# Kernel optimization log

Hardware: AMD Instinct MI355X
Metric: run time of the kernel (lower is better)

The kernel has to match this reference:

```python
import jax, jax.numpy as jnp
import numpy as np

BETA = 0.25


def setup_inputs() -> dict:
    key = jax.random.key(0)
    k1, k2 = jax.random.split(key)
    x = jax.random.normal(k1, (4, 4096, 256), dtype=jnp.float32)
    emb = jax.random.normal(k2, (8192, 256), dtype=jnp.float32)
    return {"x": x, "emb": emb}


def reference(x, emb):
    B, C, D = x.shape
    xf = x.reshape(-1, D)  # [B*C, D]
    # squared euclidean distances (argmin-equivalent to torch.cdist p=2)
    # dist2[i, n] = ||xf_i||^2 - 2 xf_i . e_n + ||e_n||^2
    dist2 = (
        jnp.sum(xf * xf, axis=-1, keepdims=True)
        - 2.0 * jnp.einsum("td,nd->tn", xf, emb)
        + jnp.sum(emb * emb, axis=-1)[None, :]
    )  # [B*C, N]
    idx = jnp.argmin(dist2, axis=-1)  # [B*C]
    quant = emb[idx]  # [B*C, D]
    commitment_loss = jnp.mean((jax.lax.stop_gradient(quant) - xf) ** 2)
    codebook_loss = jnp.mean((quant - jax.lax.stop_gradient(xf)) ** 2)
    quantize_loss = codebook_loss + BETA * commitment_loss
    # straight-through estimator
    quant_out = xf + jax.lax.stop_gradient(quant - xf)
    quant_out = quant_out.reshape(B, C, D)
    indices = idx.reshape(B, C)
    return quant_out, quantize_loss, indices
```

## Files before the change

kernel.cpp:

```cpp
#include <hip/hip_runtime.h>
#include <stdint.h>

#define T_ROWS 16384
#define D_DIM  256
#define N_CODES 8192
#define NSPLIT 4
#define NS (N_CODES / NSPLIT)
#define NCHUNK (NS / 128)
#define NITER (NCHUNK * 8)

typedef _Float16 h8v __attribute__((ext_vector_type(8)));
typedef float f4v __attribute__((ext_vector_type(4)));
typedef unsigned short u16;
typedef unsigned int u32;
typedef unsigned long long u64;

typedef const __attribute__((address_space(1))) uint32_t* as1_t;
typedef __attribute__((address_space(3))) uint32_t* as3_t;

__device__ __forceinline__ void gload_lds16(const void* g, void* l) {
    __builtin_amdgcn_global_load_lds((as1_t)(uintptr_t)g, (as3_t)(uintptr_t)l, 16, 0, 0);
}
__device__ __forceinline__ u32 umin32(u32 a, u32 b) { return a < b ? a : b; }
__device__ __forceinline__ u32 umax32(u32 a, u32 b) { return a > b ? a : b; }

__global__ void k_prep_emb(const float* __restrict__ emb, u16* __restrict__ Ef,
                           float* __restrict__ enormP) {
    int wv = threadIdx.x >> 6, lane = threadIdx.x & 63;
    int row = blockIdx.x * 4 + wv;
    float4 v = *reinterpret_cast<const float4*>(emb + (size_t)row * D_DIM + lane * 4);
    float s = v.x * v.x + v.y * v.y + v.z * v.z + v.w * v.w;
    ushort4 h;
    { _Float16 t0=(_Float16)v.x,t1=(_Float16)v.y,t2=(_Float16)v.z,t3=(_Float16)v.w;
      h.x=*reinterpret_cast<u16*>(&t0); h.y=*reinterpret_cast<u16*>(&t1);
      h.z=*reinterpret_cast<u16*>(&t2); h.w=*reinterpret_cast<u16*>(&t3); }
    reinterpret_cast<ushort4*>(Ef + (size_t)row * D_DIM)[lane] = h;
#pragma unroll
    for (int off = 32; off; off >>= 1) s += __shfl_xor(s, off, 64);
    if (lane == 0) enormP[row] = s + 1024.0f;
}

__global__ __launch_bounds__(256, 2)
void k_main_mfma(const float* __restrict__ x, const u16* __restrict__ Ef,
                 const float* __restrict__ enormP, u32* __restrict__ cand) {
    __shared__ u16 Bs[3][4096];

    const int tid = threadIdx.x;
    const int lane = tid & 63;
    const int w = tid >> 6;
    const int c15 = lane & 15, grp = lane >> 4;
    const int m0 = (int)(blockIdx.x >> 2) * 128;
    const int split = (int)(blockIdx.x & 3);
    const int nbase = split * NS;

    int boff[8];
#pragma unroll
    for (int ni = 0; ni < 8; ++ni) {
        int r = ni * 16 + c15;
        boff[ni] = (r * 64 + grp * 16) ^ (((r >> 1) & 3) << 4);
    }
    const int srow = tid >> 2;
    const int kkb = ((tid & 3) ^ ((srow >> 1) & 3)) * 8;

    h8v a[2][8];
#pragma unroll
    for (int mi = 0; mi < 2; ++mi)
#pragma unroll
        for (int ks = 0; ks < 8; ++ks) {
            const float* p = x + (size_t)(m0 + w * 32 + mi * 16 + c15) * D_DIM + ks * 32 + grp * 8;
            float4 u0 = *reinterpret_cast<const float4*>(p);
            float4 u1 = *reinterpret_cast<const float4*>(p + 4);
            h8v av;
            av[0] = (_Float16)u0.x; av[1] = (_Float16)u0.y;
            av[2] = (_Float16)u0.z; av[3] = (_Float16)u0.w;
            av[4] = (_Float16)u1.x; av[5] = (_Float16)u1.y;
            av[6] = (_Float16)u1.z; av[7] = (_Float16)u1.w;
            a[mi][ks] = av;
        }

    auto stageB = [&](int buf, int it) {
        const int nc = it >> 3, ks = it & 7;
        const u16* src = Ef + (size_t)(nbase + nc * 128 + srow) * D_DIM + ks * 32 + kkb;
        gload_lds16(src, (char*)Bs + buf * 8192 + tid * 16);
        gload_lds16(src + 64 * D_DIM, (char*)Bs + buf * 8192 + 4096 + tid * 16);
    };

    u32 b1[8], b2[8];
#pragma unroll
    for (int l = 0; l < 8; ++l) { b1[l] = 0xFFFFFFFFu; b2[l] = 0xFFFFFFFFu; }

    stageB(0, 0);
    stageB(1, 1);
    asm volatile("s_waitcnt vmcnt(2)\n\ts_barrier" ::: "memory");

    f4v acc[2][8];
    float en[8];
    int rb = 0;

    for (int nc = 0; nc < NCHUNK; ++nc) {
#pragma unroll
        for (int ni = 0; ni < 8; ++ni)
            en[ni] = enormP[nbase + nc * 128 + ni * 16 + c15];
#pragma unroll
        for (int mi = 0; mi < 2; ++mi)
#pragma unroll
            for (int ni = 0; ni < 8; ++ni) acc[mi][ni] = f4v{0.f, 0.f, 0.f, 0.f};

#pragma unroll
        for (int ks = 0; ks < 8; ++ks) {
            const int it = nc * 8 + ks;
            const int wb = rb >= 1 ? rb - 1 : 2;
            if (it < NITER - 2) stageB(wb, it + 2);

            h8v b[8];
            const char* bsb = (const char*)Bs + rb * 8192;
#pragma unroll
            for (int ni = 0; ni < 8; ++ni)
                b[ni] = *reinterpret_cast<const h8v*>(bsb + boff[ni]);

            __builtin_amdgcn_s_setprio(1);
#pragma unroll
            for (int mi = 0; mi < 2; ++mi)
#pragma unroll
                for (int ni = 0; ni < 8; ++ni)
                    acc[mi][ni] = __builtin_amdgcn_mfma_f32_16x16x32_f16(
                        a[mi][ks], b[ni], acc[mi][ni], 0, 0, 0);
            __builtin_amdgcn_s_setprio(0);

            if (ks == 7) {
#pragma unroll
                for (int mi = 0; mi < 2; ++mi)
#pragma unroll
                    for (int r = 0; r < 4; ++r) {
                        const int l = mi * 4 + r;
                        u32 kmin = 0xFFFFFFFFu;
#pragma unroll
                        for (int ni = 0; ni < 8; ++ni) {
                            float s = fmaf(-2.0f, acc[mi][ni][r], en[ni]);
                            u32 k = (__float_as_uint(s) & 0xFFFFF800u)
                                  | (u32)(nc * 128 + ni * 16 + c15);
                            kmin = umin32(kmin, k);
                        }
                        b2[l] = umin32(b2[l], umax32(b1[l], kmin));
                        b1[l] = umin32(b1[l], kmin);
                    }
            }

            if (it < NITER - 2)
                asm volatile("s_waitcnt vmcnt(2)\n\ts_barrier" ::: "memory");
            else if (it == NITER - 2)
                asm volatile("s_waitcnt vmcnt(0)\n\ts_barrier" ::: "memory");
            rb = rb < 2 ? rb + 1 : 0;
        }
    }

#pragma unroll
    for (int l = 0; l < 8; ++l) {
#pragma unroll
        for (int off = 1; off < 16; off <<= 1) {
            u32 o1 = __shfl_xor(b1[l], off, 64);
            u32 o2 = __shfl_xor(b2[l], off, 64);
            b2[l] = umin32(umax32(b1[l], o1), umin32(b2[l], o2));
            b1[l] = umin32(b1[l], o1);
        }
    }
    if (c15 == 0) {
#pragma unroll
        for (int mi = 0; mi < 2; ++mi)
#pragma unroll
            for (int r = 0; r < 4; ++r) {
                const int l = mi * 4 + r;
                const int grow = m0 + w * 32 + mi * 16 + grp * 4 + r;
                cand[grow * 8 + split * 2 + 0] = (u32)nbase + (b1[l] & 0x7FFu);
                cand[grow * 8 + split * 2 + 1] = (u32)nbase + (b2[l] & 0x7FFu);
            }
    }
}

__global__ void k_refine(const float* __restrict__ x, const float* __restrict__ emb,
                         const u32* __restrict__ cand, float* __restrict__ out,
                         double* __restrict__ partials) {
    const int tid = threadIdx.x;
    const int wv = tid >> 6, lane = tid & 63;
    const int row = blockIdx.x * 4 + wv;
    const int cslot = lane >> 3, sub = lane & 7;
    int idx = (int)cand[row * 8 + cslot];
    double d = 0.0;
#pragma unroll
    for (int j = 0; j < 8; ++j) {
        float4 xv = *reinterpret_cast<const float4*>(x + (size_t)row * D_DIM + sub * 32 + j * 4);
        float4 ev = *reinterpret_cast<const float4*>(emb + (size_t)idx * D_DIM + sub * 32 + j * 4);
        double d0 = (double)xv.x - (double)ev.x;
        double d1 = (double)xv.y - (double)ev.y;
        double d2 = (double)xv.z - (double)ev.z;
        double d3 = (double)xv.w - (double)ev.w;
        d += d0 * d0 + d1 * d1 + d2 * d2 + d3 * d3;
    }
#pragma unroll
    for (int off = 1; off < 8; off <<= 1) d += __shfl_xor(d, off, 64);
#pragma unroll
    for (int off = 8; off < 64; off <<= 1) {
        double od = __shfl_xor(d, off, 64);
        int oi = __shfl_xor(idx, off, 64);
        bool better = (od < d) || (od == d && oi < idx);
        d = better ? od : d;
        idx = better ? oi : idx;
    }
    if (lane == 0) {
        out[(size_t)T_ROWS * D_DIM + 1 + row] = (float)idx;
        partials[row] = d;
    }
    float4 e = *reinterpret_cast<const float4*>(emb + (size_t)idx * D_DIM + lane * 4);
    *reinterpret_cast<float4*>(out + (size_t)row * D_DIM + lane * 4) = e;
}

__global__ void k_loss_d(const double* __restrict__ partials, float* __restrict__ out) {
    double s = 0.0;
    const int t = threadIdx.x;
#pragma unroll
    for (int i = 0; i < 64; ++i) s += partials[t + 256 * i];
#pragma unroll
    for (int off = 32; off; off >>= 1) s += __shfl_xor(s, off, 64);
    __shared__ double sm[4];
    const int wv = t >> 6, lane = t & 63;
    if (lane == 0) sm[wv] = s;
    __syncthreads();
    if (t == 0) {
        const double tot = sm[0] + sm[1] + sm[2] + sm[3];
        out[(size_t)T_ROWS * D_DIM] = (float)(1.25 * tot / (double)((size_t)T_ROWS * D_DIM));
    }
}

__global__ void k_enorm(const float* __restrict__ emb, float* __restrict__ enorm) {
    int wave = threadIdx.x >> 6, lane = threadIdx.x & 63;
    int row = blockIdx.x * 4 + wave;
    float4 v = *reinterpret_cast<const float4*>(emb + (size_t)row * D_DIM + lane * 4);
    float s = v.x * v.x + v.y * v.y + v.z * v.z + v.w * v.w;
#pragma unroll
    for (int off = 32; off; off >>= 1) s += __shfl_xor(s, off, 64);
    if (lane == 0) enorm[row] = s;
}

__global__ void k_init(u64* __restrict__ keys) {
    keys[blockIdx.x * blockDim.x + threadIdx.x] = ~0ull;
}

__global__ __launch_bounds__(256, 2)
void k_main_fp32(const float* __restrict__ x, const float* __restrict__ emb,
                 const float* __restrict__ enorm, u64* __restrict__ keys) {
    __shared__ float Xs[32][128];
    __shared__ float Es[32][128];
    __shared__ u64 red[128][16];

    const int tid = threadIdx.x;
    const int tx = tid & 15, ty = tid >> 4;
    const int m0 = (blockIdx.x >> 2) * 128;
    const int nbase = (blockIdx.x & 3) * (N_CODES / 4);

    float best[8];
    int bidx[8];
#pragma unroll
    for (int r = 0; r < 8; ++r) { best[r] = 3.4e38f; bidx[r] = 0; }

    for (int nc = 0; nc < (N_CODES / 4) / 128; ++nc) {
        const int n0 = nbase + nc * 128;
        float acc[8][8] = {};
        for (int k0 = 0; k0 < D_DIM; k0 += 32) {
            __syncthreads();
            {
                const int m = tid & 127, q = tid >> 7;
#pragma unroll
                for (int i = 0; i < 4; ++i) {
                    const int k4 = q * 4 + i * 8;
                    float4 v = *reinterpret_cast<const float4*>(
                        x + (size_t)(m0 + m) * D_DIM + k0 + k4);
                    Xs[k4 + 0][m] = v.x; Xs[k4 + 1][m] = v.y;
                    Xs[k4 + 2][m] = v.z; Xs[k4 + 3][m] = v.w;
                }
            }
            {
                const int kq = (tid & 7) * 4, nrow = tid >> 3;
#pragma unroll
                for (int i = 0; i < 4; ++i) {
                    const int n = i * 32 + nrow;
                    float4 v = *reinterpret_cast<const float4*>(
                        emb + (size_t)(n0 + n) * D_DIM + k0 + kq);
                    const int c = n ^ kq;
                    Es[kq + 0][c] = v.x; Es[kq + 1][c] = v.y;
                    Es[kq + 2][c] = v.z; Es[kq + 3][c] = v.w;
                }
            }
            __syncthreads();
#pragma unroll
            for (int kkx = 0; kkx < 32; ++kkx) {
                const int swz = kkx & 28;
                float4 xa = *reinterpret_cast<const float4*>(&Xs[kkx][ty * 4]);
                float4 xb = *reinterpret_cast<const float4*>(&Xs[kkx][64 + ty * 4]);
                const int cb = (tx * 4) ^ swz;
                float4 ea = *reinterpret_cast<const float4*>(&Es[kkx][cb]);
                float4 eb = *reinterpret_cast<const float4*>(&Es[kkx][64 + cb]);
                float xr[8] = {xa.x, xa.y, xa.z, xa.w, xb.x, xb.y, xb.z, xb.w};
                float ec[8] = {ea.x, ea.y, ea.z, ea.w, eb.x, eb.y, eb.z, eb.w};
#pragma unroll
                for (int r = 0; r < 8; ++r)
#pragma unroll
                    for (int c = 0; c < 8; ++c)
                        acc[r][c] = fmaf(xr[r], ec[c], acc[r][c]);
            }
        }
#pragma unroll
        for (int c = 0; c < 8; ++c) {
            const int ncol = n0 + ((c < 4) ? (tx * 4 + c) : (64 + tx * 4 + (c - 4)));
            const float en = enorm[ncol];
#pragma unroll
            for (int r = 0; r < 8; ++r) {
                const float score = fmaf(-2.0f, acc[r][c], en);
                if (score < best[r]) { best[r] = score; bidx[r] = ncol; }
            }
        }
    }
#pragma unroll
    for (int r = 0; r < 8; ++r) {
        const int row = (r < 4) ? (ty * 4 + r) : (64 + ty * 4 + (r - 4));
        unsigned u = __float_as_uint(best[r]);
        u = (u & 0x80000000u) ? ~u : (u | 0x80000000u);
        red[row][tx] = ((u64)u << 32) | (unsigned)bidx[r];
    }
    __syncthreads();
    if (tid < 128) {
        u64 k = red[tid][0];
#pragma unroll
        for (int t = 1; t < 16; ++t) { u64 v = red[tid][t]; k = (v < k) ? v : k; }
        atomicMin(&keys[m0 + tid], k);
    }
}

__global__ void k_out_fb(const float* __restrict__ x, const float* __restrict__ emb,
                         const u64* __restrict__ keys, float* __restrict__ out,
                         float* __restrict__ partials) {
    const int tid = threadIdx.x;
    const int m0 = blockIdx.x * 64;
    __shared__ int idx_s[64];
    if (tid < 64) {
        const u32 idx = (u32)keys[m0 + tid];
        idx_s[tid] = (int)idx;
        out[(size_t)T_ROWS * D_DIM + 1 + m0 + tid] = (float)idx;
    }
    __syncthreads();
    const int wave = tid >> 6, lane = tid & 63;
    float loss = 0.f;
#pragma unroll
    for (int i = 0; i < 16; ++i) {
        const int r = i * 4 + wave;
        const int row = m0 + r;
        const int idx = idx_s[r];
        float4 e  = *reinterpret_cast<const float4*>(emb + (size_t)idx * D_DIM + lane * 4);
        float4 xv = *reinterpret_cast<const float4*>(x + (size_t)row * D_DIM + lane * 4);
        *reinterpret_cast<float4*>(out + (size_t)row * D_DIM + lane * 4) = e;
        const float dx = e.x - xv.x, dy = e.y - xv.y, dz = e.z - xv.z, dw = e.w - xv.w;
        loss += dx * dx + dy * dy + dz * dz + dw * dw;
    }
#pragma unroll
    for (int off = 32; off; off >>= 1) loss += __shfl_xor(loss, off, 64);
    __shared__ float wl[4];
    if (lane == 0) wl[wave] = loss;
    __syncthreads();
    if (tid == 0) partials[blockIdx.x] = wl[0] + wl[1] + wl[2] + wl[3];
}

__global__ void k_loss_f(const float* __restrict__ partials, float* __restrict__ out) {
    double s = (double)partials[threadIdx.x];
#pragma unroll
    for (int off = 32; off; off >>= 1) s += __shfl_xor(s, off, 64);
    __shared__ double sm[4];
    const int wave = threadIdx.x >> 6, lane = threadIdx.x & 63;
    if (lane == 0) sm[wave] = s;
    __syncthreads();
    if (threadIdx.x == 0) {
        const double tot = sm[0] + sm[1] + sm[2] + sm[3];
        out[(size_t)T_ROWS * D_DIM] = (float)(1.25 * tot / (double)((size_t)T_ROWS * D_DIM));
    }
}

extern "C" void kernel_launch(void* const* d_in, const int* in_sizes, int n_in,
                              void* d_out, int out_size, void* d_ws, size_t ws_size,
                              hipStream_t stream) {
    const float* x = (const float*)d_in[0];
    const float* emb = (const float*)d_in[1];
    float* out = (float*)d_out;
    char* ws = (char*)d_ws;

    const size_t NEED = 4867072ull;
    if (ws_size >= NEED) {
        u16* Ef = (u16*)(ws + 0);
        float* enormP = (float*)(ws + 4194304);
        u32* cand = (u32*)(ws + 4227072);
        double* partials = (double*)(ws + 4751360);

        k_prep_emb<<<N_CODES / 4, 256, 0, stream>>>(emb, Ef, enormP);
        k_main_mfma<<<(T_ROWS / 128) * NSPLIT, 256, 0, stream>>>(x, Ef, enormP, cand);
        k_refine<<<T_ROWS / 4, 256, 0, stream>>>(x, emb, cand, out, partials);
        k_loss_d<<<1, 256, 0, stream>>>(partials, out);
    } else {
        float* enorm = (float*)(ws + 0);
        u64* keys = (u64*)(ws + 32768);
        float* partials = (float*)(ws + 163840);

        k_enorm<<<N_CODES / 4, 256, 0, stream>>>(emb, enorm);
        k_init<<<T_ROWS / 256, 256, 0, stream>>>(keys);
        k_main_fp32<<<(T_ROWS / 128) * 4, 256, 0, stream>>>(x, emb, enorm, keys);
        k_out_fb<<<T_ROWS / 64, 256, 0, stream>>>(x, emb, keys, out, partials);
        k_loss_f<<<1, 256, 0, stream>>>(partials, out);
    }
}
```

Before: 122.8 us.

## Deepen B-tile pipeline to four LDS buffers with register double-buffered fragments

Result: faster. 119.2 us, median of 2 (-2.9%).

```diff
diff --git a/kernel.cpp b/kernel.cpp
--- a/kernel.cpp
+++ b/kernel.cpp
@@ -43,7 +43,7 @@
 __global__ __launch_bounds__(256, 2)
 void k_main_mfma(const float* __restrict__ x, const u16* __restrict__ Ef,
                  const float* __restrict__ enormP, u32* __restrict__ cand) {
-    __shared__ u16 Bs[3][4096];
+    __shared__ u16 Bs[4][4096];
 
     const int tid = threadIdx.x;
     const int lane = tid & 63;
@@ -91,66 +91,76 @@
 
     stageB(0, 0);
     stageB(1, 1);
-    asm volatile("s_waitcnt vmcnt(2)\n\ts_barrier" ::: "memory");
+    stageB(2, 2);
+    asm volatile("s_waitcnt vmcnt(4)\n\ts_barrier" ::: "memory");
+
+    h8v bcur[8], bnxt[8];
+#pragma unroll
+    for (int ni = 0; ni < 8; ++ni)
+        bcur[ni] = *reinterpret_cast<const h8v*>((const char*)Bs + boff[ni]);
 
     f4v acc[2][8];
     float en[8];
-    int rb = 0;
+
+    auto do_step = [&](int it, int ks, h8v (&bc)[8], h8v (&bn)[8]) {
+        asm volatile("s_waitcnt vmcnt(2)\n\ts_barrier" ::: "memory");
+        {
+            int it3 = it + 3;
+            if (it3 > NITER - 1) it3 = NITER - 1;
+            stageB((it + 3) & 3, it3);
+        }
+        if (ks == 0) {
+            const int nc = it >> 3;
+#pragma unroll
+            for (int ni = 0; ni < 8; ++ni)
+                en[ni] = enormP[nbase + nc * 128 + ni * 16 + c15];
+        }
+        {
+            const char* bsb = (const char*)Bs + ((it + 1) & 3) * 8192;
+#pragma unroll
+            for (int ni = 0; ni < 8; ++ni)
+                bn[ni] = *reinterpret_cast<const h8v*>(bsb + boff[ni]);
+        }
+        __builtin_amdgcn_s_setprio(1);
+#pragma unroll
+        for (int mi = 0; mi < 2; ++mi)
+#pragma unroll
+            for (int ni = 0; ni < 8; ++ni)
+                acc[mi][ni] = __builtin_amdgcn_mfma_f32_16x16x32_f16(
+                    a[mi][ks], bc[ni], acc[mi][ni], 0, 0, 0);
+        __builtin_amdgcn_s_setprio(0);
+
+        if (ks == 7) {
+            const int nc = it >> 3;
+#pragma unroll
+            for (int mi = 0; mi < 2; ++mi)
+#pragma unroll
+                for (int r = 0; r < 4; ++r) {
+                    const int l = mi * 4 + r;
+                    u32 kmin = 0xFFFFFFFFu;
+#pragma unroll
+                    for (int ni = 0; ni < 8; ++ni) {
+                        float s = fmaf(-2.0f, acc[mi][ni][r], en[ni]);
+                        u32 k = (__float_as_uint(s) & 0xFFFFF800u)
+                              | (u32)(nc * 128 + ni * 16 + c15);
+                        kmin = umin32(kmin, k);
+                    }
+                    b2[l] = umin32(b2[l], umax32(b1[l], kmin));
+                    b1[l] = umin32(b1[l], kmin);
+                }
+        }
+    };
 
     for (int nc = 0; nc < NCHUNK; ++nc) {
 #pragma unroll
-        for (int ni = 0; ni < 8; ++ni)
-            en[ni] = enormP[nbase + nc * 128 + ni * 16 + c15];
-#pragma unroll
         for (int mi = 0; mi < 2; ++mi)
 #pragma unroll
             for (int ni = 0; ni < 8; ++ni) acc[mi][ni] = f4v{0.f, 0.f, 0.f, 0.f};
 
 #pragma unroll
-        for (int ks = 0; ks < 8; ++ks) {
-            const int it = nc * 8 + ks;
-            const int wb = rb >= 1 ? rb - 1 : 2;
-            if (it < NITER - 2) stageB(wb, it + 2);
-
-            h8v b[8];
-            const char* bsb = (const char*)Bs + rb * 8192;
-#pragma unroll
-            for (int ni = 0; ni < 8; ++ni)
-                b[ni] = *reinterpret_cast<const h8v*>(bsb + boff[ni]);
-
-            __builtin_amdgcn_s_setprio(1);
-#pragma unroll
-            for (int mi = 0; mi < 2; ++mi)
-#pragma unroll
-                for (int ni = 0; ni < 8; ++ni)
-                    acc[mi][ni] = __builtin_amdgcn_mfma_f32_16x16x32_f16(
-                        a[mi][ks], b[ni], acc[mi][ni], 0, 0, 0);
-            __builtin_amdgcn_s_setprio(0);
-
-            if (ks == 7) {
-#pragma unroll
-                for (int mi = 0; mi < 2; ++mi)
-#pragma unroll
-                    for (int r = 0; r < 4; ++r) {
-                        const int l = mi * 4 + r;
-                        u32 kmin = 0xFFFFFFFFu;
-#pragma unroll
-                        for (int ni = 0; ni < 8; ++ni) {
-                            float s = fmaf(-2.0f, acc[mi][ni][r], en[ni]);
-                            u32 k = (__float_as_uint(s) & 0xFFFFF800u)
-                                  | (u32)(nc * 128 + ni * 16 + c15);
-                            kmin = umin32(kmin, k);
-                        }
-                        b2[l] = umin32(b2[l], umax32(b1[l], kmin));
-                        b1[l] = umin32(b1[l], kmin);
-                    }
-            }
-
-            if (it < NITER - 2)
-                asm volatile("s_waitcnt vmcnt(2)\n\ts_barrier" ::: "memory");
-            else if (it == NITER - 2)
-                asm volatile("s_waitcnt vmcnt(0)\n\ts_barrier" ::: "memory");
-            rb = rb < 2 ? rb + 1 : 0;
+        for (int kp = 0; kp < 4; ++kp) {
+            do_step(nc * 8 + kp * 2 + 0, kp * 2 + 0, bcur, bnxt);
+            do_step(nc * 8 + kp * 2 + 1, kp * 2 + 1, bnxt, bcur);
         }
     }
 
```
